# Performance work log

Measured on AMD Instinct MI355X. Metric: run time of the kernel, lower is better.

The kernel has to match this reference:

```python
import jax, jax.numpy as jnp
import numpy as np

TEMP = 0.0005

def conv1d(x, w, b):
    # x: [B, Cin, T], w: [Cout, Cin, K] -> [B, Cout, T] with SAME padding
    out = jax.lax.conv_general_dilated(x, w, (1,), 'SAME', dimension_numbers=('NCH', 'OIH', 'NCH'))
    return out + b[None, :, None]

def setup_inputs() -> dict:
    key = jax.random.key(0)
    ks = jax.random.split(key, 24)
    B, Cs, T1 = 16, 80, 1000   # spec channels / mel frames
    Ct, T2 = 512, 200          # text channels / phonemes
    Ca, G = 80, 256            # attention channels / speaker embedding
    n = lambda i, shape: jax.random.normal(ks[i], shape, jnp.float32)
    w = lambda i, shape: n(i, shape) * 0.05
    return {
        'queries': n(0, (B, Cs, T1)),
        'keys': n(1, (B, Ct, T2)),
        'mask': jnp.ones((B, T2), jnp.int32),
        'attn_prior': jax.random.uniform(ks[2], (B, T1, T2), jnp.float32),
        'g': n(3, (B, G)),
        # key_proj: Conv(Ct -> 2Ct, k=3) -> ReLU -> Conv(2Ct -> Ca, k=1)
        'wk1': w(4, (2 * Ct, Ct, 3)), 'bk1': jnp.zeros((2 * Ct,), jnp.float32),
        'wk2': w(5, (Ca, 2 * Ct, 1)), 'bk2': jnp.zeros((Ca,), jnp.float32),
        # query_proj: Conv(Cs -> 2Cs, k=3) -> ReLU -> Conv(2Cs -> Cs, k=1) -> ReLU -> Conv(Cs -> Ca, k=1)
        'wq1': w(6, (2 * Cs, Cs, 3)), 'bq1': jnp.zeros((2 * Cs,), jnp.float32),
        'wq2': w(7, (Cs, 2 * Cs, 1)), 'bq2': jnp.zeros((Cs,), jnp.float32),
        'wq3': w(8, (Ca, Cs, 1)), 'bq3': jnp.zeros((Ca,), jnp.float32),
        # speaker projections (LinearNorm): gin -> n_text_channels / n_spec_channels
        'w_kspk': w(9, (Ct, G)), 'b_kspk': jnp.zeros((Ct,), jnp.float32),
        'w_qspk': w(10, (Cs, G)), 'b_qspk': jnp.zeros((Cs,), jnp.float32),
    }

def reference(queries, keys, mask, attn_prior, g, wk1, bk1, wk2, bk2, wq1, bq1, wq2, bq2, wq3, bq3, w_kspk, b_kspk, w_qspk, b_qspk):
    # speaker conditioning: same projected vector added at every time step
    keys = keys + (g @ w_kspk.T + b_kspk)[:, :, None]
    queries = queries + (g @ w_qspk.T + b_qspk)[:, :, None]
    # projections
    k_enc = conv1d(jax.nn.relu(conv1d(keys, wk1, bk1)), wk2, bk2)              # [B, Ca, T2]
    q = jax.nn.relu(conv1d(queries, wq1, bq1))
    q = jax.nn.relu(conv1d(q, wq2, bq2))
    q_enc = conv1d(q, wq3, bq3)                                                # [B, Ca, T1]
    # squared L2 distance via GEMM trick: |q|^2 + |k|^2 - 2 q.k  (same math as broadcast diff)
    q2 = jnp.sum(q_enc * q_enc, axis=1)[:, :, None]                            # [B, T1, 1]
    k2 = jnp.sum(k_enc * k_enc, axis=1)[:, None, :]                            # [B, 1, T2]
    qk = jnp.einsum('bct,bcs->bts', q_enc, k_enc)                              # [B, T1, T2]
    attn = (-TEMP * (q2 + k2 - 2.0 * qk))[:, None]                             # [B, 1, T1, T2]
    attn = jax.nn.log_softmax(attn, axis=3) + jnp.log(attn_prior[:, None] + 1e-8)
    attn_logprob = attn
    neg_inf = jnp.where(mask[:, None, None, :] == 0, -jnp.inf, 0.0)
    attn = jax.nn.softmax(attn + neg_inf, axis=3)
    return attn, attn_logprob
```

## Files before the change

### kernel.cpp

```cpp
#include <hip/hip_runtime.h>
#include <hip/hip_bf16.h>
#include <math.h>

#define NB 16
#define CS 80
#define T1 1000
#define CT 512
#define T2 200
#define CA 80
#define GD 256
#define C2T 1024
#define C2S 160
#define TEMP_F 0.0005f
#define ENC_STR 96

typedef __attribute__((ext_vector_type(8))) short short8;
typedef __attribute__((ext_vector_type(4))) float floatx4;

__device__ __forceinline__ short f2bf(float x) {
    unsigned u = __builtin_bit_cast(unsigned, x);
    unsigned r = (u + 0x7fffu + ((u >> 16) & 1u)) >> 16;
    return (short)r;
}

template <int COUT, int CIN, int KW, int COP, int CINP>
__device__ __forceinline__ void wpack_body(const float* __restrict__ w,
                                           short* __restrict__ wp, int bid) {
    constexpr int NC32 = CINP / 32;
    constexpr int NFRAG = (COP / 16) * KW * NC32;
    int gid = bid * 256 + threadIdx.x;
    int frag = gid >> 6, lane = gid & 63;
    if (frag >= NFRAG) return;
    int co16 = frag / (KW * NC32), rem = frag - co16 * (KW * NC32);
    int k = rem / NC32, ci32 = rem - k * NC32;
    int co = co16 * 16 + (lane & 15);
    int ci = ci32 * 32 + (lane >> 4) * 8;
    short8 v;
#pragma unroll
    for (int j = 0; j < 8; j++) {
        float f = 0.f;
        if (co < COUT && ci + j < CIN) f = w[((size_t)co * CIN + ci + j) * KW + k];
        v[j] = f2bf(f);
    }
    *(short8*)(wp + (size_t)frag * 512 + lane * 8) = v;
}

template <int C, int T>
__device__ __forceinline__ void addspkT_body(const float* __restrict__ in,
                                             const float* __restrict__ g,
                                             const float* __restrict__ w_spk,
                                             const float* __restrict__ b_spk,
                                             short* __restrict__ outT,
                                             float* sm, int bx, int by, int b) {
    float* spkS = sm;
    float* S = sm + 32;
    const int t0 = bx * 64, c0 = by * 32;
    const int tid = threadIdx.x;
    int cl = tid >> 3, part = tid & 7;
    int c = c0 + cl;
    float s = 0.f;
    if (c < C) {
        const float* wr = w_spk + (size_t)c * GD;
        const float* gr = g + b * GD;
        int j0 = part * 32;
#pragma unroll
        for (int j = 0; j < 32; j++) s += gr[j0 + j] * wr[j0 + j];
    }
    s += __shfl_xor(s, 1, 64); s += __shfl_xor(s, 2, 64); s += __shfl_xor(s, 4, 64);
    if (part == 0) spkS[cl] = s + ((c < C) ? b_spk[c] : 0.f);
    __syncthreads();
    for (int i = tid; i < 32 * 64; i += 256) {
        int cll = i >> 6, tl = i & 63;
        int gc = c0 + cll, gt = t0 + tl;
        float v = 0.f;
        if (gc < C && gt < T) v = in[((size_t)b * C + gc) * T + gt] + spkS[cll];
        S[cll * 65 + tl] = v;
    }
    __syncthreads();
    for (int i = tid; i < 64 * 32; i += 256) {
        int tl = i >> 5, cll = i & 31;
        int gt = t0 + tl, gc = c0 + cll;
        if (gc < C && gt < T) outT[((size_t)b * T + gt) * C + gc] = f2bf(S[cll * 65 + tl]);
    }
}

__global__ __launch_bounds__(256) void prep_kernel(
    const float* __restrict__ keys, const float* __restrict__ queries, const float* __restrict__ g,
    const float* __restrict__ wk1, const float* __restrict__ wq1, const float* __restrict__ wk2,
    const float* __restrict__ wq2, const float* __restrict__ wq3,
    const float* __restrict__ w_kspk, const float* __restrict__ b_kspk,
    const float* __restrict__ w_qspk, const float* __restrict__ b_qspk,
    short* __restrict__ wk1p, short* __restrict__ wq1p, short* __restrict__ wk2p,
    short* __restrict__ wq2p, short* __restrict__ wq3p,
    short* __restrict__ xkT, short* __restrict__ xqT) {
    __shared__ float sm[32 + 32 * 65];
    int bid = blockIdx.x;
    if (bid < 768) { wpack_body<C2T, CT, 3, C2T, CT>(wk1, wk1p, bid); return; }
    bid -= 768;
    if (bid < 27) { wpack_body<C2S, CS, 3, 192, 96>(wq1, wq1p, bid); return; }
    bid -= 27;
    if (bid < 40) { wpack_body<CA, C2T, 1, 80, 1024>(wk2, wk2p, bid); return; }
    bid -= 40;
    if (bid < 7) { wpack_body<CA, C2S, 1, 80, 160>(wq2, wq2p, bid); return; }
    bid -= 7;
    if (bid < 4) { wpack_body<CA, CS, 1, 80, 96>(wq3, wq3p, bid); return; }
    bid -= 4;
    if (bid < 1024) {
        int bx = bid & 3, by = (bid >> 2) & 15, b = bid >> 6;
        addspkT_body<CT, T2>(keys, g, w_kspk, b_kspk, xkT, sm, bx, by, b);
        return;
    }
    bid -= 1024;
    {
        int bx = bid & 15, by = (bid >> 4) % 3, b = bid / 48;
        addspkT_body<CS, T1>(queries, g, w_qspk, b_qspk, xqT, sm, bx, by, b);
    }
}

template <int CIN, int COUT, int T, int KW, bool RELU, int CICH, int NC32T>
__device__ __forceinline__ void conv_body(const short* __restrict__ xT,
                                          const short* __restrict__ wp,
                                          const float* __restrict__ bias,
                                          short* __restrict__ outT,
                                          short* Xs, int bx, int by, int b) {
    constexpr int TT = 128, COT = 64;
    constexpr int PAD = KW / 2;
    constexpr int XROWS = TT + KW - 1;
    constexpr int PITCH = CICH + 8;
    constexpr int NPC = CICH / 8;
    constexpr int NC32 = CICH / 32;
    constexpr int CINP = NC32T * 32;
    constexpr int NCHK = CINP / CICH;
    constexpr int NPIECE = XROWS * NPC;
    constexpr int NLD = (NPIECE + 255) / 256;

    const int t0 = bx * TT, co0 = by * COT;
    const int tid = threadIdx.x, wave = tid >> 6, lane = tid & 63;
    const int quad = lane >> 4, l16 = lane & 15;
    const int wt = wave * 32;
    const int co16_0 = co0 >> 4;
    const short* xb = xT + (size_t)b * T * CIN;

    floatx4 acc[4][2];
#pragma unroll
    for (int mi = 0; mi < 4; mi++)
#pragma unroll
        for (int ni = 0; ni < 2; ni++) acc[mi][ni] = (floatx4){0.f, 0.f, 0.f, 0.f};

    for (int i = tid; i < NPIECE; i += 256) {
        int r = i / NPC, p = i - r * NPC;
        int t = t0 + r - PAD, ci = p * 8;
        uint4 v = {0u, 0u, 0u, 0u};
        if ((unsigned)t < (unsigned)T && ci + 8 <= CIN)
            v = *(const uint4*)(xb + (size_t)t * CIN + ci);
        *(uint4*)(Xs + r * PITCH + p * 8) = v;
    }
    __syncthreads();

    for (int kc = 0; kc < NCHK; kc++) {
        uint4 tmp[NLD];
        if (NCHK > 1 && kc + 1 < NCHK) {
            int ci0n = (kc + 1) * CICH;
#pragma unroll
            for (int ld = 0; ld < NLD; ld++) {
                int i = tid + ld * 256;
                tmp[ld] = (uint4){0u, 0u, 0u, 0u};
                if (i < NPIECE) {
                    int r = i / NPC, p = i - r * NPC;
                    int t = t0 + r - PAD, ci = ci0n + p * 8;
                    if ((unsigned)t < (unsigned)T && ci + 8 <= CIN)
                        tmp[ld] = *(const uint4*)(xb + (size_t)t * CIN + ci);
                }
            }
        }
        const short* Xb = Xs + (NCHK > 1 ? (kc & 1) : 0) * XROWS * PITCH;
#pragma unroll
        for (int k = 0; k < KW; k++) {
#pragma unroll
            for (int kk = 0; kk < NC32; kk++) {
                int ci32 = kc * NC32 + kk;
                short8 a[4];
#pragma unroll
                for (int mi = 0; mi < 4; mi++)
                    a[mi] = *(const short8*)(wp +
                        ((size_t)((co16_0 + mi) * KW + k) * NC32T + ci32) * 512 + lane * 8);
#pragma unroll
                for (int ni = 0; ni < 2; ni++) {
                    short8 bb = *(const short8*)(Xb + (wt + ni * 16 + l16 + k) * PITCH +
                                                 kk * 32 + quad * 8);
#pragma unroll
                    for (int mi = 0; mi < 4; mi++)
                        acc[mi][ni] = __builtin_amdgcn_mfma_f32_16x16x32_bf16(a[mi], bb,
                                                                              acc[mi][ni], 0, 0, 0);
                }
            }
        }
        if (NCHK > 1 && kc + 1 < NCHK) {
            short* Xn = Xs + ((kc + 1) & 1) * XROWS * PITCH;
#pragma unroll
            for (int ld = 0; ld < NLD; ld++) {
                int i = tid + ld * 256;
                if (i < NPIECE) {
                    int r = i / NPC, p = i - r * NPC;
                    *(uint4*)(Xn + r * PITCH + p * 8) = tmp[ld];
                }
            }
            __syncthreads();
        }
    }
#pragma unroll
    for (int mi = 0; mi < 4; mi++) {
        int cb = co0 + mi * 16 + quad * 4;
        if (cb < COUT) {
            float4 bv = *(const float4*)(bias + cb);
#pragma unroll
            for (int ni = 0; ni < 2; ni++) {
                int t = t0 + wt + ni * 16 + l16;
                if (t < T) {
                    float v0 = acc[mi][ni][0] + bv.x, v1 = acc[mi][ni][1] + bv.y;
                    float v2 = acc[mi][ni][2] + bv.z, v3 = acc[mi][ni][3] + bv.w;
                    if (RELU) {
                        v0 = fmaxf(v0, 0.f); v1 = fmaxf(v1, 0.f);
                        v2 = fmaxf(v2, 0.f); v3 = fmaxf(v3, 0.f);
                    }
                    ushort4 o;
                    o.x = (unsigned short)f2bf(v0); o.y = (unsigned short)f2bf(v1);
                    o.z = (unsigned short)f2bf(v2); o.w = (unsigned short)f2bf(v3);
                    *(ushort4*)(outT + ((size_t)b * T + t) * COUT + cb) = o;
                }
            }
        }
    }
}

__global__ __launch_bounds__(256, 2) void conv_kernel(
    const short* __restrict__ xkT, const short* __restrict__ wk1p,
    const float* __restrict__ bk1, short* __restrict__ kh1T,
    const short* __restrict__ xqT, const short* __restrict__ wq1p,
    const float* __restrict__ bq1, short* __restrict__ qh1T) {
    __shared__ short sm[18720];
    int bid = blockIdx.x;
    if (bid < 512) {
        int bx = bid & 1, by = (bid >> 1) & 15, b = bid >> 5;
        conv_body<CT, C2T, T2, 3, true, 64, 16>(xkT, wk1p, bk1, kh1T, sm, bx, by, b);
    } else {
        int r = bid - 512;
        int bx = r & 7, by = (r >> 3) % 3, b = r / 24;
        conv_body<CS, C2S, T1, 3, true, 96, 3>(xqT, wq1p, bq1, qh1T, sm, bx, by, b);
    }
}

__device__ __forceinline__ void kgemm_body(const short* __restrict__ xT,
                                           const short* __restrict__ wp,
                                           const float* __restrict__ bias,
                                           short* __restrict__ outT,
                                           float* __restrict__ k2ws,
                                           short* sm, int bid) {
    constexpr int K = 1024, KCH = 128, PITCH = 136, NPC = 16, NCHK = 8;
    const int n0 = bid * 64;
    const int tid = threadIdx.x, wave = tid >> 6, lane = tid & 63;
    const int quad = lane >> 4, l16 = lane & 15;
    floatx4 acc[5];
#pragma unroll
    for (int mi = 0; mi < 5; mi++) acc[mi] = (floatx4){0.f, 0.f, 0.f, 0.f};

    for (int i = tid; i < 64 * NPC; i += 256) {
        int r = i / NPC, p = i - r * NPC;
        *(uint4*)(sm + r * PITCH + p * 8) = *(const uint4*)(xT + (size_t)(n0 + r) * K + p * 8);
    }
    __syncthreads();
    for (int kc = 0; kc < NCHK; kc++) {
        uint4 tmp[4];
        if (kc + 1 < NCHK) {
            int ci0 = (kc + 1) * KCH;
#pragma unroll
            for (int ld = 0; ld < 4; ld++) {
                int i = tid + ld * 256;
                int r = i / NPC, p = i - r * NPC;
                tmp[ld] = *(const uint4*)(xT + (size_t)(n0 + r) * K + ci0 + p * 8);
            }
        }
        const short* Xb = sm + (kc & 1) * 64 * PITCH;
#pragma unroll
        for (int kk = 0; kk < 4; kk++) {
            int ci32 = kc * 4 + kk;
            short8 bb = *(const short8*)(Xb + (wave * 16 + l16) * PITCH + kk * 32 + quad * 8);
#pragma unroll
            for (int mi = 0; mi < 5; mi++) {
                short8 a = *(const short8*)(wp + ((size_t)(mi * 32 + ci32)) * 512 + lane * 8);
                acc[mi] = __builtin_amdgcn_mfma_f32_16x16x32_bf16(a, bb, acc[mi], 0, 0, 0);
            }
        }
        if (kc + 1 < NCHK) {
            short* Xn = sm + ((kc + 1) & 1) * 64 * PITCH;
#pragma unroll
            for (int ld = 0; ld < 4; ld++) {
                int i = tid + ld * 256;
                int r = i / NPC, p = i - r * NPC;
                *(uint4*)(Xn + r * PITCH + p * 8) = tmp[ld];
            }
            __syncthreads();
        }
    }
    int n = n0 + wave * 16 + l16;
    float sq = 0.f;
#pragma unroll
    for (int mi = 0; mi < 5; mi++) {
        int cb = mi * 16 + quad * 4;
        float4 bv = *(const float4*)(bias + cb);
        float v0 = acc[mi][0] + bv.x, v1 = acc[mi][1] + bv.y;
        float v2 = acc[mi][2] + bv.z, v3 = acc[mi][3] + bv.w;
        sq += v0 * v0 + v1 * v1 + v2 * v2 + v3 * v3;
        ushort4 o;
        o.x = (unsigned short)f2bf(v0); o.y = (unsigned short)f2bf(v1);
        o.z = (unsigned short)f2bf(v2); o.w = (unsigned short)f2bf(v3);
        *(ushort4*)(outT + (size_t)n * ENC_STR + cb) = o;
    }
    if (quad < 2) *(uint4*)(outT + (size_t)n * ENC_STR + 80 + quad * 8) = (uint4){0u, 0u, 0u, 0u};
    sq += __shfl_xor(sq, 16, 64);
    sq += __shfl_xor(sq, 32, 64);
    if (quad == 0) k2ws[n] = sq;
}

__device__ __forceinline__ void qconv23_body(const short* __restrict__ h1,
                                             const short* __restrict__ w2p,
                                             const float* __restrict__ b2,
                                             const short* __restrict__ w3p,
                                             const float* __restrict__ b3,
                                             short* __restrict__ outT, short* sm, int bid) {
    constexpr int K1 = 160, P1 = 168, NPC1 = 20, P3 = 104;
    short* Xs = sm;
    short* Hs = sm + 64 * P1;
    const int n0 = bid * 64;
    const int tid = threadIdx.x, wave = tid >> 6, lane = tid & 63;
    const int quad = lane >> 4, l16 = lane & 15;

    for (int i = tid; i < 64 * NPC1; i += 256) {
        int r = i / NPC1, p = i - r * NPC1;
        *(uint4*)(Xs + r * P1 + p * 8) = *(const uint4*)(h1 + (size_t)(n0 + r) * K1 + p * 8);
    }
    if (tid < 128) *(uint4*)(Hs + (tid >> 1) * P3 + 80 + (tid & 1) * 8) = (uint4){0u, 0u, 0u, 0u};
    __syncthreads();

    floatx4 acc[5];
#pragma unroll
    for (int mi = 0; mi < 5; mi++) acc[mi] = (floatx4){0.f, 0.f, 0.f, 0.f};
#pragma unroll
    for (int kk = 0; kk < 5; kk++) {
        short8 bb = *(const short8*)(Xs + (wave * 16 + l16) * P1 + kk * 32 + quad * 8);
#pragma unroll
        for (int mi = 0; mi < 5; mi++) {
            short8 a = *(const short8*)(w2p + ((size_t)(mi * 5 + kk)) * 512 + lane * 8);
            acc[mi] = __builtin_amdgcn_mfma_f32_16x16x32_bf16(a, bb, acc[mi], 0, 0, 0);
        }
    }
#pragma unroll
    for (int mi = 0; mi < 5; mi++) {
        int cb = mi * 16 + quad * 4;
        float4 bv = *(const float4*)(b2 + cb);
        ushort4 o;
        o.x = (unsigned short)f2bf(fmaxf(acc[mi][0] + bv.x, 0.f));
        o.y = (unsigned short)f2bf(fmaxf(acc[mi][1] + bv.y, 0.f));
        o.z = (unsigned short)f2bf(fmaxf(acc[mi][2] + bv.z, 0.f));
        o.w = (unsigned short)f2bf(fmaxf(acc[mi][3] + bv.w, 0.f));
        *(ushort4*)(Hs + (wave * 16 + l16) * P3 + cb) = o;
    }
    __syncthreads();

    floatx4 acc3[5];
#pragma unroll
    for (int mi = 0; mi < 5; mi++) acc3[mi] = (floatx4){0.f, 0.f, 0.f, 0.f};
#pragma unroll
    for (int kk = 0; kk < 3; kk++) {
        short8 bb = *(const short8*)(Hs + (wave * 16 + l16) * P3 + kk * 32 + quad * 8);
#pragma unroll
        for (int mi = 0; mi < 5; mi++) {
            short8 a = *(const short8*)(w3p + ((size_t)(mi * 3 + kk)) * 512 + lane * 8);
            acc3[mi] = __builtin_amdgcn_mfma_f32_16x16x32_bf16(a, bb, acc3[mi], 0, 0, 0);
        }
    }
    int n = n0 + wave * 16 + l16;
#pragma unroll
    for (int mi = 0; mi < 5; mi++) {
        int cb = mi * 16 + quad * 4;
        float4 bv = *(const float4*)(b3 + cb);
        ushort4 o;
        o.x = (unsigned short)f2bf(acc3[mi][0] + bv.x);
        o.y = (unsigned short)f2bf(acc3[mi][1] + bv.y);
        o.z = (unsigned short)f2bf(acc3[mi][2] + bv.z);
        o.w = (unsigned short)f2bf(acc3[mi][3] + bv.w);
        *(ushort4*)(outT + (size_t)n * ENC_STR + cb) = o;
    }
    if (quad < 2) *(uint4*)(outT + (size_t)n * ENC_STR + 80 + quad * 8) = (uint4){0u, 0u, 0u, 0u};
}

__global__ __launch_bounds__(256, 2) void gemm_kernel(
    const short* __restrict__ kh1T, const short* __restrict__ wk2p,
    const float* __restrict__ bk2, short* __restrict__ k_encT, float* __restrict__ k2ws,
    const short* __restrict__ qh1T, const short* __restrict__ wq2p,
    const float* __restrict__ bq2, const short* __restrict__ wq3p,
    const float* __restrict__ bq3, short* __restrict__ q_encT) {
    __shared__ short sm[17408];
    int bid = blockIdx.x;
    if (bid < 50) kgemm_body(kh1T, wk2p, bk2, k_encT, k2ws, sm, bid);
    else qconv23_body(qh1T, wq2p, bq2, wq3p, bq3, q_encT, sm, bid - 50);
}

__device__ __forceinline__ float rmax16(float v) {
#pragma unroll
    for (int o = 1; o < 16; o <<= 1) v = fmaxf(v, __shfl_xor(v, o, 64));
    return v;
}
__device__ __forceinline__ float rsum16(float v) {
#pragma unroll
    for (int o = 1; o < 16; o <<= 1) v += __shfl_xor(v, o, 64);
    return v;
}

__global__ __launch_bounds__(256) void attn_kernel(const short* __restrict__ q_encT,
                                                   const short* __restrict__ k_encT,
                                                   const float* __restrict__ k2ws,
                                                   const float* __restrict__ prior,
                                                   const int* __restrict__ mask,
                                                   float* __restrict__ out_attn,
                                                   float* __restrict__ out_logp) {
    const int t10 = blockIdx.x * 64, b = blockIdx.y;
    const int tid = threadIdx.x, wave = tid >> 6, lane = tid & 63;
    const int quad = lane >> 4, l16 = lane & 15;

    float k2v[13]; int mskv[13];
#pragma unroll
    for (int n = 0; n < 13; n++) {
        int t2 = n * 16 + l16, t2c = t2 < T2 ? t2 : T2 - 1;
        k2v[n] = k2ws[b * T2 + t2c];
        mskv[n] = (t2 < T2) ? mask[b * T2 + t2] : 0;
    }
    const int t1base = t10 + wave * 16 + quad * 4;
    float pr[4][13];
#pragma unroll
    for (int r = 0; r < 4; r++) {
        int t1 = t1base + r, t1c = t1 < T1 ? t1 : T1 - 1;
#pragma unroll
        for (int n = 0; n < 13; n++) {
            int t2 = n * 16 + l16, t2c = t2 < T2 ? t2 : T2 - 1;
            pr[r][n] = prior[((size_t)b * T1 + t1c) * T2 + t2c];
        }
    }

    floatx4 acc[13];
#pragma unroll
    for (int n = 0; n < 13; n++) acc[n] = (floatx4){0.f, 0.f, 0.f, 0.f};
    const short* qb = q_encT + ((size_t)(b * T1 + t10 + wave * 16 + l16)) * ENC_STR + quad * 8;
    const short* kb = k_encT + ((size_t)(b * T2 + l16)) * ENC_STR + quad * 8;
#pragma unroll
    for (int kk = 0; kk < 3; kk++) {
        short8 a = *(const short8*)(qb + kk * 32);
#pragma unroll
        for (int n = 0; n < 13; n++) {
            short8 bb = *(const short8*)(kb + (size_t)n * 16 * ENC_STR + kk * 32);
            acc[n] = __builtin_amdgcn_mfma_f32_16x16x32_bf16(a, bb, acc[n], 0, 0, 0);
        }
    }

#pragma unroll
    for (int r = 0; r < 4; r++) {
        int t1 = t1base + r;
        bool t1ok = t1 < T1;
        float s[13], u[13];
        float mx = -INFINITY, mxu = -INFINITY;
#pragma unroll
        for (int n = 0; n < 13; n++) {
            int t2 = n * 16 + l16;
            float sv = (t2 < T2) ? TEMP_F * (2.f * acc[n][r] - k2v[n]) : -INFINITY;
            s[n] = sv;
            float uv = (t2 < T2) ? sv + __logf(pr[r][n] + 1e-8f) : -INFINITY;
            u[n] = uv;
            mx = fmaxf(mx, sv);
            mxu = fmaxf(mxu, (mskv[n] != 0) ? uv : -INFINITY);
        }
        float m = rmax16(mx);
        float m2 = rmax16(mxu);
        float se = 0.f, se2 = 0.f;
        float e2v[13];
#pragma unroll
        for (int n = 0; n < 13; n++) {
            se += (s[n] == -INFINITY) ? 0.f : __expf(s[n] - m);
            float e2 = (mskv[n] != 0) ? __expf(u[n] - m2) : 0.f;
            e2v[n] = e2;
            se2 += e2;
        }
        float logZ = __logf(rsum16(se));
        float invZ2 = 1.f / rsum16(se2);
        if (t1ok) {
#pragma unroll
            for (int n = 0; n < 13; n++) {
                int t2 = n * 16 + l16;
                if (t2 < T2) {
                    size_t o = ((size_t)b * T1 + t1) * T2 + t2;
                    out_attn[o] = e2v[n] * invZ2;
                    out_logp[o] = u[n] - m - logZ;
                }
            }
        }
    }
}

extern "C" void kernel_launch(void* const* d_in, const int* in_sizes, int n_in,
                              void* d_out, int out_size, void* d_ws, size_t ws_size,
                              hipStream_t stream) {
    const float* queries = (const float*)d_in[0];
    const float* keys    = (const float*)d_in[1];
    const int*   mask    = (const int*)d_in[2];
    const float* prior   = (const float*)d_in[3];
    const float* g       = (const float*)d_in[4];
    const float* wk1 = (const float*)d_in[5];
    const float* bk1 = (const float*)d_in[6];
    const float* wk2 = (const float*)d_in[7];
    const float* bk2 = (const float*)d_in[8];
    const float* wq1 = (const float*)d_in[9];
    const float* bq1 = (const float*)d_in[10];
    const float* wq2 = (const float*)d_in[11];
    const float* bq2 = (const float*)d_in[12];
    const float* wq3 = (const float*)d_in[13];
    const float* bq3 = (const float*)d_in[14];
    const float* w_kspk = (const float*)d_in[15];
    const float* b_kspk = (const float*)d_in[16];
    const float* w_qspk = (const float*)d_in[17];
    const float* b_qspk = (const float*)d_in[18];

    short* wsS   = (short*)d_ws;
    short* xkT   = wsS;
    short* xqT   = wsS + 1638400;
    short* wk1p  = wsS + 2918400;
    short* wq1p  = wsS + 4491264;
    short* wk2p  = wsS + 4546560;
    short* wq2p  = wsS + 4628480;
    short* wq3p  = wsS + 4641280;
    short* k_encT = wsS + 4648960;
    short* q_encT = wsS + 4957696;
    float* k2ws  = (float*)d_ws + 3248384;
    short* doS  = (short*)d_out;
    short* kh1T = doS;
    short* qh1T = doS + 3276800;

    prep_kernel<<<dim3(2638), dim3(256), 0, stream>>>(
        keys, queries, g, wk1, wq1, wk2, wq2, wq3,
        w_kspk, b_kspk, w_qspk, b_qspk,
        wk1p, wq1p, wk2p, wq2p, wq3p, xkT, xqT);
    conv_kernel<<<dim3(896), dim3(256), 0, stream>>>(xkT, wk1p, bk1, kh1T,
                                                     xqT, wq1p, bq1, qh1T);
    gemm_kernel<<<dim3(300), dim3(256), 0, stream>>>(kh1T, wk2p, bk2, k_encT, k2ws,
                                                     qh1T, wq2p, bq2, wq3p, bq3, q_encT);
    float* out_attn = (float*)d_out;
    float* out_logp = out_attn + (size_t)NB * T1 * T2;
    attn_kernel<<<dim3(16, NB), dim3(256), 0, stream>>>(q_encT, k_encT, k2ws, prior, mask,
                                                        out_attn, out_logp);
}
```

Baseline: 190.5 us.

## Read conv/GEMM B operands directly from padded global buffers instead of LDS staging

The transposed activation buffers are written with zero halo rows and padded channel strides, so the conv and 1x1 GEMM bodies can load MFMA B fragments straight from global memory (L1/L2) instead of staging tiles through LDS with double buffering and barriers. This removes shared memory use and __syncthreads, and raises the launch-bounds occupancy hint to 3 blocks. In exchange it relies on cache hits for the reused rows across the kernel taps, adds extra zeroing blocks to prep, and changes the workspace layout.

Result: slower. 209.8 us (+10.1%).

```diff
diff --git a/kernel.cpp b/kernel.cpp
--- a/kernel.cpp
+++ b/kernel.cpp
@@ -13,6 +13,8 @@
 #define C2S 160
 #define TEMP_F 0.0005f
 #define ENC_STR 96
+#define TPK 258
+#define TPQ 1027
 
 typedef __attribute__((ext_vector_type(8))) short short8;
 typedef __attribute__((ext_vector_type(4))) float floatx4;
@@ -45,7 +47,7 @@
     *(short8*)(wp + (size_t)frag * 512 + lane * 8) = v;
 }
 
-template <int C, int T>
+template <int C, int T, int CP, int TP>
 __device__ __forceinline__ void addspkT_body(const float* __restrict__ in,
                                              const float* __restrict__ g,
                                              const float* __restrict__ w_spk,
@@ -80,7 +82,8 @@
     for (int i = tid; i < 64 * 32; i += 256) {
         int tl = i >> 5, cll = i & 31;
         int gt = t0 + tl, gc = c0 + cll;
-        if (gc < C && gt < T) outT[((size_t)b * T + gt) * C + gc] = f2bf(S[cll * 65 + tl]);
+        if (gc < CP && gt < T)
+            outT[((size_t)b * TP + gt + 1) * CP + gc] = f2bf(S[cll * 65 + tl]);
     }
 }
 
@@ -92,7 +95,7 @@
     const float* __restrict__ w_qspk, const float* __restrict__ b_qspk,
     short* __restrict__ wk1p, short* __restrict__ wq1p, short* __restrict__ wk2p,
     short* __restrict__ wq2p, short* __restrict__ wq3p,
-    short* __restrict__ xkT, short* __restrict__ xqT) {
+    short* __restrict__ xkTp, short* __restrict__ xqTp) {
     __shared__ float sm[32 + 32 * 65];
     int bid = blockIdx.x;
     if (bid < 768) { wpack_body<C2T, CT, 3, C2T, CT>(wk1, wk1p, bid); return; }
@@ -107,39 +110,53 @@
     bid -= 4;
     if (bid < 1024) {
         int bx = bid & 3, by = (bid >> 2) & 15, b = bid >> 6;
-        addspkT_body<CT, T2>(keys, g, w_kspk, b_kspk, xkT, sm, bx, by, b);
+        addspkT_body<CT, T2, 512, TPK>(keys, g, w_kspk, b_kspk, xkTp, sm, bx, by, b);
         return;
     }
     bid -= 1024;
+    if (bid < 768) {
+        int bx = bid & 15, by = (bid >> 4) % 3, b = bid / 48;
+        addspkT_body<CS, T1, ENC_STR, TPQ>(queries, g, w_qspk, b_qspk, xqTp, sm, bx, by, b);
+        return;
+    }
+    bid -= 768;
+    if (bid < 32) {
+        const uint4 z = {0u, 0u, 0u, 0u};
+        for (int i = bid * 256 + threadIdx.x; i < 16 * 3712; i += 32 * 256) {
+            int b = i / 3712, r = i - b * 3712;
+            int r64 = r >> 6, c8 = r & 63;
+            int row = (r64 == 0) ? 0 : 200 + r64;
+            *(uint4*)(xkTp + ((size_t)b * TPK + row) * 512 + c8 * 8) = z;
+        }
+        return;
+    }
+    bid -= 32;
     {
-        int bx = bid & 15, by = (bid >> 4) % 3, b = bid / 48;
-        addspkT_body<CS, T1>(queries, g, w_qspk, b_qspk, xqT, sm, bx, by, b);
-    }
-}
-
-template <int CIN, int COUT, int T, int KW, bool RELU, int CICH, int NC32T>
+        const uint4 z = {0u, 0u, 0u, 0u};
+        for (int i = bid * 256 + threadIdx.x; i < 16 * 324; i += 4 * 256) {
+            int b = i / 324, r = i - b * 324;
+            int r12 = r / 12, c8 = r - r12 * 12;
+            int row = (r12 == 0) ? 0 : 1000 + r12;
+            *(uint4*)(xqTp + ((size_t)b * TPQ + row) * ENC_STR + c8 * 8) = z;
+        }
+    }
+}
+
+template <int COUT, int T, int KW, bool RELU, int CICH, int NC32T, int TP>
 __device__ __forceinline__ void conv_body(const short* __restrict__ xT,
                                           const short* __restrict__ wp,
                                           const float* __restrict__ bias,
                                           short* __restrict__ outT,
-                                          short* Xs, int bx, int by, int b) {
-    constexpr int TT = 128, COT = 64;
-    constexpr int PAD = KW / 2;
-    constexpr int XROWS = TT + KW - 1;
-    constexpr int PITCH = CICH + 8;
-    constexpr int NPC = CICH / 8;
+                                          int bx, int by, int b) {
+    constexpr int STRIDE = NC32T * 32;
     constexpr int NC32 = CICH / 32;
-    constexpr int CINP = NC32T * 32;
-    constexpr int NCHK = CINP / CICH;
-    constexpr int NPIECE = XROWS * NPC;
-    constexpr int NLD = (NPIECE + 255) / 256;
-
-    const int t0 = bx * TT, co0 = by * COT;
+    constexpr int NCHK = STRIDE / CICH;
+    const int t0 = bx * 128, co0 = by * 64;
     const int tid = threadIdx.x, wave = tid >> 6, lane = tid & 63;
     const int quad = lane >> 4, l16 = lane & 15;
     const int wt = wave * 32;
     const int co16_0 = co0 >> 4;
-    const short* xb = xT + (size_t)b * T * CIN;
+    const short* xb = xT + ((size_t)b * TP + t0 + wt + l16) * STRIDE + quad * 8;
 
     floatx4 acc[4][2];
 #pragma unroll
@@ -147,33 +164,7 @@
 #pragma unroll
         for (int ni = 0; ni < 2; ni++) acc[mi][ni] = (floatx4){0.f, 0.f, 0.f, 0.f};
 
-    for (int i = tid; i < NPIECE; i += 256) {
-        int r = i / NPC, p = i - r * NPC;
-        int t = t0 + r - PAD, ci = p * 8;
-        uint4 v = {0u, 0u, 0u, 0u};
-        if ((unsigned)t < (unsigned)T && ci + 8 <= CIN)
-            v = *(const uint4*)(xb + (size_t)t * CIN + ci);
-        *(uint4*)(Xs + r * PITCH + p * 8) = v;
-    }
-    __syncthreads();
-
     for (int kc = 0; kc < NCHK; kc++) {
-        uint4 tmp[NLD];
-        if (NCHK > 1 && kc + 1 < NCHK) {
-            int ci0n = (kc + 1) * CICH;
-#pragma unroll
-            for (int ld = 0; ld < NLD; ld++) {
-                int i = tid + ld * 256;
-                tmp[ld] = (uint4){0u, 0u, 0u, 0u};
-                if (i < NPIECE) {
-                    int r = i / NPC, p = i - r * NPC;
-                    int t = t0 + r - PAD, ci = ci0n + p * 8;
-                    if ((unsigned)t < (unsigned)T && ci + 8 <= CIN)
-                        tmp[ld] = *(const uint4*)(xb + (size_t)t * CIN + ci);
-                }
-            }
-        }
-        const short* Xb = Xs + (NCHK > 1 ? (kc & 1) : 0) * XROWS * PITCH;
 #pragma unroll
         for (int k = 0; k < KW; k++) {
 #pragma unroll
@@ -186,26 +177,14 @@
                         ((size_t)((co16_0 + mi) * KW + k) * NC32T + ci32) * 512 + lane * 8);
 #pragma unroll
                 for (int ni = 0; ni < 2; ni++) {
-                    short8 bb = *(const short8*)(Xb + (wt + ni * 16 + l16 + k) * PITCH +
-                                                 kk * 32 + quad * 8);
+                    short8 bb = *(const short8*)(xb + (size_t)(ni * 16 + k) * STRIDE +
+                                                 kc * CICH + kk * 32);
 #pragma unroll
                     for (int mi = 0; mi < 4; mi++)
                         acc[mi][ni] = __builtin_amdgcn_mfma_f32_16x16x32_bf16(a[mi], bb,
                                                                               acc[mi][ni], 0, 0, 0);
                 }
             }
-        }
-        if (NCHK > 1 && kc + 1 < NCHK) {
-            short* Xn = Xs + ((kc + 1) & 1) * XROWS * PITCH;
-#pragma unroll
-            for (int ld = 0; ld < NLD; ld++) {
-                int i = tid + ld * 256;
-                if (i < NPIECE) {
-                    int r = i / NPC, p = i - r * NPC;
-                    *(uint4*)(Xn + r * PITCH + p * 8) = tmp[ld];
-                }
-            }
-            __syncthreads();
         }
     }
 #pragma unroll
@@ -233,20 +212,19 @@
     }
 }
 
-__global__ __launch_bounds__(256, 2) void conv_kernel(
-    const short* __restrict__ xkT, const short* __restrict__ wk1p,
+__global__ __launch_bounds__(256, 3) void conv_kernel(
+    const short* __restrict__ xkTp, const short* __restrict__ wk1p,
     const float* __restrict__ bk1, short* __restrict__ kh1T,
-    const short* __restrict__ xqT, const short* __restrict__ wq1p,
+    const short* __restrict__ xqTp, const short* __restrict__ wq1p,
     const float* __restrict__ bq1, short* __restrict__ qh1T) {
-    __shared__ short sm[18720];
     int bid = blockIdx.x;
     if (bid < 512) {
         int bx = bid & 1, by = (bid >> 1) & 15, b = bid >> 5;
-        conv_body<CT, C2T, T2, 3, true, 64, 16>(xkT, wk1p, bk1, kh1T, sm, bx, by, b);
+        conv_body<C2T, T2, 3, true, 64, 16, TPK>(xkTp, wk1p, bk1, kh1T, bx, by, b);
     } else {
         int r = bid - 512;
         int bx = r & 7, by = (r >> 3) % 3, b = r / 24;
-        conv_body<CS, C2S, T1, 3, true, 96, 3>(xqT, wq1p, bq1, qh1T, sm, bx, by, b);
+        conv_body<C2S, T1, 3, true, 96, 3, TPQ>(xqTp, wq1p, bq1, qh1T, bx, by, b);
     }
 }
 
@@ -254,52 +232,24 @@
                                            const short* __restrict__ wp,
                                            const float* __restrict__ bias,
                                            short* __restrict__ outT,
-                                           float* __restrict__ k2ws,
-                                           short* sm, int bid) {
-    constexpr int K = 1024, KCH = 128, PITCH = 136, NPC = 16, NCHK = 8;
+                                           float* __restrict__ k2ws, int bid) {
     const int n0 = bid * 64;
     const int tid = threadIdx.x, wave = tid >> 6, lane = tid & 63;
     const int quad = lane >> 4, l16 = lane & 15;
+    const short* xrow = xT + (size_t)(n0 + wave * 16 + l16) * 1024 + quad * 8;
     floatx4 acc[5];
 #pragma unroll
     for (int mi = 0; mi < 5; mi++) acc[mi] = (floatx4){0.f, 0.f, 0.f, 0.f};
-
-    for (int i = tid; i < 64 * NPC; i += 256) {
-        int r = i / NPC, p = i - r * NPC;
-        *(uint4*)(sm + r * PITCH + p * 8) = *(const uint4*)(xT + (size_t)(n0 + r) * K + p * 8);
-    }
-    __syncthreads();
-    for (int kc = 0; kc < NCHK; kc++) {
-        uint4 tmp[4];
-        if (kc + 1 < NCHK) {
-            int ci0 = (kc + 1) * KCH;
-#pragma unroll
-            for (int ld = 0; ld < 4; ld++) {
-                int i = tid + ld * 256;
-                int r = i / NPC, p = i - r * NPC;
-                tmp[ld] = *(const uint4*)(xT + (size_t)(n0 + r) * K + ci0 + p * 8);
-            }
-        }
-        const short* Xb = sm + (kc & 1) * 64 * PITCH;
+    for (int kc = 0; kc < 8; kc++) {
 #pragma unroll
         for (int kk = 0; kk < 4; kk++) {
             int ci32 = kc * 4 + kk;
-            short8 bb = *(const short8*)(Xb + (wave * 16 + l16) * PITCH + kk * 32 + quad * 8);
+            short8 bb = *(const short8*)(xrow + ci32 * 32);
 #pragma unroll
             for (int mi = 0; mi < 5; mi++) {
                 short8 a = *(const short8*)(wp + ((size_t)(mi * 32 + ci32)) * 512 + lane * 8);
                 acc[mi] = __builtin_amdgcn_mfma_f32_16x16x32_bf16(a, bb, acc[mi], 0, 0, 0);
             }
-        }
-        if (kc + 1 < NCHK) {
-            short* Xn = sm + ((kc + 1) & 1) * 64 * PITCH;
-#pragma unroll
-            for (int ld = 0; ld < 4; ld++) {
-                int i = tid + ld * 256;
-                int r = i / NPC, p = i - r * NPC;
-                *(uint4*)(Xn + r * PITCH + p * 8) = tmp[ld];
-            }
-            __syncthreads();
         }
     }
     int n = n0 + wave * 16 + l16;
@@ -327,27 +277,22 @@
                                              const float* __restrict__ b2,
                                              const short* __restrict__ w3p,
                                              const float* __restrict__ b3,
-                                             short* __restrict__ outT, short* sm, int bid) {
-    constexpr int K1 = 160, P1 = 168, NPC1 = 20, P3 = 104;
-    short* Xs = sm;
-    short* Hs = sm + 64 * P1;
+                                             short* __restrict__ outT,
+                                             short* Hs, int bid) {
+    constexpr int P3 = 104;
     const int n0 = bid * 64;
     const int tid = threadIdx.x, wave = tid >> 6, lane = tid & 63;
     const int quad = lane >> 4, l16 = lane & 15;
-
-    for (int i = tid; i < 64 * NPC1; i += 256) {
-        int r = i / NPC1, p = i - r * NPC1;
-        *(uint4*)(Xs + r * P1 + p * 8) = *(const uint4*)(h1 + (size_t)(n0 + r) * K1 + p * 8);
-    }
+    const short* xrow = h1 + (size_t)(n0 + wave * 16 + l16) * 160 + quad * 8;
+
     if (tid < 128) *(uint4*)(Hs + (tid >> 1) * P3 + 80 + (tid & 1) * 8) = (uint4){0u, 0u, 0u, 0u};
-    __syncthreads();
 
     floatx4 acc[5];
 #pragma unroll
     for (int mi = 0; mi < 5; mi++) acc[mi] = (floatx4){0.f, 0.f, 0.f, 0.f};
 #pragma unroll
     for (int kk = 0; kk < 5; kk++) {
-        short8 bb = *(const short8*)(Xs + (wave * 16 + l16) * P1 + kk * 32 + quad * 8);
+        short8 bb = *(const short8*)(xrow + kk * 32);
 #pragma unroll
         for (int mi = 0; mi < 5; mi++) {
             short8 a = *(const short8*)(w2p + ((size_t)(mi * 5 + kk)) * 512 + lane * 8);
@@ -394,16 +339,16 @@
     if (quad < 2) *(uint4*)(outT + (size_t)n * ENC_STR + 80 + quad * 8) = (uint4){0u, 0u, 0u, 0u};
 }
 
-__global__ __launch_bounds__(256, 2) void gemm_kernel(
+__global__ __launch_bounds__(256, 3) void gemm_kernel(
     const short* __restrict__ kh1T, const short* __restrict__ wk2p,
     const float* __restrict__ bk2, short* __restrict__ k_encT, float* __restrict__ k2ws,
     const short* __restrict__ qh1T, const short* __restrict__ wq2p,
     const float* __restrict__ bq2, const short* __restrict__ wq3p,
     const float* __restrict__ bq3, short* __restrict__ q_encT) {
-    __shared__ short sm[17408];
+    __shared__ short Hs[64 * 104];
     int bid = blockIdx.x;
-    if (bid < 50) kgemm_body(kh1T, wk2p, bk2, k_encT, k2ws, sm, bid);
-    else qconv23_body(qh1T, wq2p, bq2, wq3p, bq3, q_encT, sm, bid - 50);
+    if (bid < 50) kgemm_body(kh1T, wk2p, bk2, k_encT, k2ws, bid);
+    else qconv23_body(qh1T, wq2p, bq2, wq3p, bq3, q_encT, Hs, bid - 50);
 }
 
 __device__ __forceinline__ float rmax16(float v) {
@@ -529,26 +474,26 @@
     const float* b_qspk = (const float*)d_in[18];
 
     short* wsS   = (short*)d_ws;
-    short* xkT   = wsS;
-    short* xqT   = wsS + 1638400;
-    short* wk1p  = wsS + 2918400;
-    short* wq1p  = wsS + 4491264;
-    short* wk2p  = wsS + 4546560;
-    short* wq2p  = wsS + 4628480;
-    short* wq3p  = wsS + 4641280;
-    short* k_encT = wsS + 4648960;
-    short* q_encT = wsS + 4957696;
-    float* k2ws  = (float*)d_ws + 3248384;
+    short* xkTp  = wsS;
+    short* xqTp  = wsS + 2113536;
+    short* wk1p  = wsS + 3691008;
+    short* wq1p  = wsS + 5263872;
+    short* wk2p  = wsS + 5319168;
+    short* wq2p  = wsS + 5401088;
+    short* wq3p  = wsS + 5413888;
+    short* k_encT = wsS + 5421568;
+    short* q_encT = wsS + 5730304;
+    float* k2ws  = (float*)d_ws + 3634688;
     short* doS  = (short*)d_out;
     short* kh1T = doS;
     short* qh1T = doS + 3276800;
 
-    prep_kernel<<<dim3(2638), dim3(256), 0, stream>>>(
+    prep_kernel<<<dim3(2674), dim3(256), 0, stream>>>(
         keys, queries, g, wk1, wq1, wk2, wq2, wq3,
         w_kspk, b_kspk, w_qspk, b_qspk,
-        wk1p, wq1p, wk2p, wq2p, wq3p, xkT, xqT);
-    conv_kernel<<<dim3(896), dim3(256), 0, stream>>>(xkT, wk1p, bk1, kh1T,
-                                                     xqT, wq1p, bq1, qh1T);
+        wk1p, wq1p, wk2p, wq2p, wq3p, xkTp, xqTp);
+    conv_kernel<<<dim3(896), dim3(256), 0, stream>>>(xkTp, wk1p, bk1, kh1T,
+                                                     xqTp, wq1p, bq1, qh1T);
     gemm_kernel<<<dim3(300), dim3(256), 0, stream>>>(kh1T, wk2p, bk2, k_encT, k2ws,
                                                      qh1T, wq2p, bq2, wq3p, bq3, q_encT);
     float* out_attn = (float*)d_out;
```
